# Kernel optimization log

Hardware: AMD Instinct MI355X
Metric: run time of the kernel (lower is better)

The kernel has to match this reference:

```python
import jax, jax.numpy as jnp
import numpy as np

NC = 80          # class_num
THRESH = 0.5     # objectness threshold (forward arg `thresh`)
IOU_T = 0.3      # NMS IoU threshold (utils.nms(boxes_c, 0.3))
K = 512          # fixed candidate budget per image (jit-safe replacement for nonzero)


def _decode(out, t, anchors):
    """_filter + _parse for one scale. out: (B, 3*(5+NC), H, W) -> boxes (B, H*W*3, 6), conf (B, H*W*3).
    Box columns: x1, y1, x2, y2, conf, cls."""
    B, C, H, W = out.shape
    o = out.transpose(0, 2, 3, 1).reshape(B, H, W, 3, 5 + NC)
    txy = jax.nn.sigmoid(o[..., 0:2])          # sigmoid on tx, ty
    conf = jax.nn.sigmoid(o[..., 4])           # sigmoid on objectness
    gy = jnp.arange(H, dtype=out.dtype)[:, None, None]   # grid row index (idxs[:,1])
    gx = jnp.arange(W, dtype=out.dtype)[None, :, None]   # grid col index (idxs[:,2])
    cy = (gy + txy[..., 1]) * t
    cx = (gx + txy[..., 0]) * t
    w = anchors[:, 0] * jnp.exp(o[..., 2])     # anchors broadcast over anchor axis
    h = anchors[:, 1] * jnp.exp(o[..., 3])
    cls = jnp.argmax(o[..., 5:], axis=-1).astype(out.dtype)
    boxes = jnp.stack([cx - w / 2, cy - h / 2, cx + w / 2, cy + h / 2, conf, cls], axis=-1)
    return boxes.reshape(B, -1, 6), conf.reshape(B, -1)


def _iou(b):
    """Pairwise IoU. b: (B, K, 4) -> (B, K, K)."""
    x1, y1, x2, y2 = b[..., 0], b[..., 1], b[..., 2], b[..., 3]
    area = (x2 - x1) * (y2 - y1)
    ix1 = jnp.maximum(x1[:, :, None], x1[:, None, :])
    iy1 = jnp.maximum(y1[:, :, None], y1[:, None, :])
    ix2 = jnp.minimum(x2[:, :, None], x2[:, None, :])
    iy2 = jnp.minimum(y2[:, :, None], y2[:, None, :])
    inter = jnp.maximum(ix2 - ix1, 0.0) * jnp.maximum(iy2 - iy1, 0.0)
    return inter / (area[:, :, None] + area[:, None, :] - inter + 1e-9)


def setup_inputs() -> dict:
    key = jax.random.key(0)
    k1, k2, k3 = jax.random.split(key, 3)
    B, C = 32, 3 * (5 + NC)
    return {
        "out13": jax.random.normal(k1, (B, C, 13, 13), jnp.float32),
        "out26": jax.random.normal(k2, (B, C, 26, 26), jnp.float32),
        "out52": jax.random.normal(k3, (B, C, 52, 52), jnp.float32),
        "anchors13": jnp.array([[116.0, 90.0], [156.0, 198.0], [373.0, 326.0]], jnp.float32),
        "anchors26": jnp.array([[30.0, 61.0], [62.0, 45.0], [59.0, 119.0]], jnp.float32),
        "anchors52": jnp.array([[10.0, 13.0], [16.0, 30.0], [33.0, 23.0]], jnp.float32),
    }


def reference(out13, out26, out52, anchors13, anchors26, anchors52):
    b13, c13 = _decode(out13, 32.0, anchors13)
    b26, c26 = _decode(out26, 16.0, anchors26)
    b52, c52 = _decode(out52, 8.0, anchors52)
    boxes = jnp.concatenate([b13, b26, b52], axis=1)   # (B, N, 6), N = 3549*3
    conf = jnp.concatenate([c13, c26, c52], axis=1)    # (B, N)
    B = boxes.shape[0]

    # threshold filter (conf > thresh) realized as masked top-K (jit-safe nonzero)
    scores = jnp.where(conf > THRESH, conf, -1.0)
    vals, idx = jax.lax.top_k(scores, K)               # sorted descending, as utils.nms expects
    bk = jnp.take_along_axis(boxes, idx[..., None], axis=1)   # (B, K, 6)
    valid = vals > THRESH                              # (B, K)

    # per-class greedy NMS
    iou = _iou(bk[..., :4])                            # (B, K, K)
    same_cls = bk[..., 5][:, :, None] == bk[..., 5][:, None, :]
    suppress = same_cls & (iou > IOU_T)

    def step(keep, i):
        sup_i = jnp.any(keep & suppress[:, i, :], axis=-1)
        keep = keep.at[:, i].set(valid[:, i] & ~sup_i)
        return keep, None

    keep, _ = jax.lax.scan(step, jnp.zeros((B, K), dtype=bool), jnp.arange(K))
    # (B, K, 7): x1, y1, x2, y2, conf, cls, keep_flag
    return jnp.concatenate([bk, keep[..., None].astype(bk.dtype)], axis=-1)
```

## Files before the change

### kernel.cpp

```cpp
#include <hip/hip_runtime.h>
#include <stdint.h>

#define NC13 507
#define NC26 2028
#define NC52 8112
#define NCAND 10647
#define KSEL 512
#define POOLCAP 4096
#define SUPW 17
#define CMW 17

__device__ __forceinline__ unsigned long long cand_key(
    int i, int b,
    const float* __restrict__ in13,
    const float* __restrict__ in26,
    const float* __restrict__ in52)
{
    const float* in; int HW, base;
    if (i < NC13)              { in = in13; HW = 169;  base = 0; }
    else if (i < NC13 + NC26)  { in = in26; HW = 676;  base = NC13; }
    else                       { in = in52; HW = 2704; base = NC13 + NC26; }
    const int within = i - base;
    const int a  = within / HW;
    const int hw = within - a * HW;
    const float xo = in[((size_t)b * 255 + (size_t)a * 85 + 4) * HW + hw];
    const int n = base + hw * 3 + a;
    const unsigned long long low = (unsigned long long)(0x3FFFu - (unsigned)n);
    return (xo > 0.0f)
        ? ((1ull << 63) | ((unsigned long long)__float_as_uint(xo) << 32) | low)
        : low;
}

__global__ __launch_bounds__(1024) void selscore_kernel(
    const float* __restrict__ in13,
    const float* __restrict__ in26,
    const float* __restrict__ in52,
    int* __restrict__ selidx,
    int* __restrict__ selv)
{
    __shared__ unsigned int hist[4096];
    __shared__ unsigned long long pool[POOLCAP];
    __shared__ unsigned int cnt;
    __shared__ unsigned long long sh_prefix;
    __shared__ unsigned long long sh_tmin;
    __shared__ int sh_krem;
    __shared__ int sh_shift;
    __shared__ int sh_break;

    const int b = blockIdx.x;
    const int tid = threadIdx.x;

    if (tid == 0) { sh_prefix = 0; sh_krem = KSEL; sh_shift = 52; sh_break = 0; cnt = 0; }
    __syncthreads();

    while (true) {
        const int shift = sh_shift;
        const unsigned long long prefix = sh_prefix;
        const int krem = sh_krem;
        __syncthreads();
        for (int i = tid; i < 4096; i += 1024) hist[i] = 0;
        __syncthreads();
        for (int i = tid; i < NCAND; i += 1024) {
            const unsigned long long k = cand_key(i, b, in13, in26, in52);
            const bool ok = (shift == 52) || ((k >> (shift + 12)) == prefix);
            if (ok) atomicAdd(&hist[(unsigned)((k >> shift) & 0xFFFull)], 1u);
        }
        __syncthreads();
        if (tid < 64) {
            unsigned int s = 0;
            for (int q = 0; q < 64; ++q) s += hist[tid * 64 + q];
            unsigned int suf = s;
            for (int off = 1; off < 64; off <<= 1) {
                const unsigned int v = __shfl_down(suf, off);
                if (tid + off < 64) suf += v;
            }
            const unsigned long long ball = __ballot(suf >= (unsigned)krem);
            const int lstar = 63 - __clzll(ball);
            const unsigned int base = (lstar < 63) ? __shfl(suf, lstar + 1) : 0u;
            const unsigned int wv = hist[lstar * 64 + (63 - tid)];
            unsigned int pv = wv;
            for (int off = 1; off < 64; off <<= 1) {
                const unsigned int v = __shfl_up(pv, off);
                if (tid >= (unsigned)off) pv += v;
            }
            const unsigned long long b2 = __ballot(base + pv >= (unsigned)krem);
            const int mstar = __ffsll(b2) - 1;
            const unsigned int pvm = __shfl(pv, mstar);
            const unsigned int wvm = __shfl(wv, mstar);
            if (tid == 0) {
                const int dstar = lstar * 64 + (63 - mstar);
                const unsigned long long np = (prefix << 12) | (unsigned long long)dstar;
                const int Albl = (int)(base + pvm - wvm);
                const int Cpool = (KSEL - krem) + Albl + (int)wvm;
                sh_prefix = np;
                sh_krem = krem - Albl;
                if (Cpool <= POOLCAP || shift == 4) {
                    sh_break = 1;
                    sh_tmin = np << shift;
                } else {
                    sh_shift = shift - 12;
                }
            }
        }
        __syncthreads();
        if (sh_break) break;
    }
    const unsigned long long tmin = sh_tmin;

    for (int i = tid; i < NCAND; i += 1024) {
        const unsigned long long k = cand_key(i, b, in13, in26, in52);
        if (k >= tmin) {
            const unsigned int p = atomicAdd(&cnt, 1u);
            if (p < POOLCAP) pool[p] = k;
        }
    }
    __syncthreads();
    const int C = ((int)cnt < POOLCAP) ? (int)cnt : POOLCAP;

    for (int p = tid; p < C; p += 1024) {
        const unsigned long long k = pool[p];
        int r = 0;
        for (int j = 0; j < C; ++j) r += (pool[j] > k) ? 1 : 0;
        if (r < KSEL) {
            const int idx = 0x3FFF - (int)(k & 0x3FFFull);
            selidx[(size_t)b * KSEL + r] = idx;
            selv[(size_t)b * KSEL + r]   = (int)(k >> 63);
        }
    }
}

__device__ __forceinline__ unsigned long long cls_key(float v, int c) {
    unsigned int u = __float_as_uint(v);
    u = (u & 0x80000000u) ? ~u : (u | 0x80000000u);
    return ((unsigned long long)u << 32) | (unsigned long long)(127 - c);
}

__global__ __launch_bounds__(256) void gather_kernel(
    const float* __restrict__ in13,
    const float* __restrict__ in26,
    const float* __restrict__ in52,
    const float* __restrict__ a13,
    const float* __restrict__ a26,
    const float* __restrict__ a52,
    const int* __restrict__ selidx,
    float* __restrict__ bk,
    int* __restrict__ bkC)
{
    const int lane = threadIdx.x & 63;
    const int r = blockIdx.x * 4 + (threadIdx.x >> 6);
    const int b = blockIdx.y;
    const int idx = selidx[(size_t)b * KSEL + r];

    const float* in; const float* anch; int H; float ts; int loc;
    if (idx < NC13)             { in = in13; anch = a13; H = 13; ts = 32.f; loc = idx; }
    else if (idx < NC13 + NC26) { in = in26; anch = a26; H = 26; ts = 16.f; loc = idx - NC13; }
    else                        { in = in52; anch = a52; H = 52; ts = 8.f;  loc = idx - NC13 - NC26; }
    const int W = H, HW = H * W;
    const int hw = loc / 3, a = loc - hw * 3;
    const int h = hw / W,  w = hw - h * W;
    const float* p = in + ((size_t)b * 255 + (size_t)a * 85) * HW + hw;

    const float v0 = p[(size_t)(5 + lane) * HW];
    const float v1 = p[(size_t)(69 + (lane & 15)) * HW];
    const float bc = p[(size_t)(lane % 5) * HW];

    unsigned long long k = cls_key(v0, lane);
    {
        const unsigned long long k1 = cls_key(v1, 64 + (lane & 15));
        if (k1 > k) k = k1;
    }
    #pragma unroll
    for (int off = 32; off; off >>= 1) {
        const unsigned int hi = __shfl_xor((unsigned int)(k >> 32), off);
        const unsigned int lo = __shfl_xor((unsigned int)(k & 0xFFFFFFFFu), off);
        const unsigned long long o = ((unsigned long long)hi << 32) | lo;
        if (o > k) k = o;
    }
    const int cls = 127 - (int)(k & 0x7Full);

    const float tx = __shfl(bc, 0);
    const float ty = __shfl(bc, 1);
    const float tw = __shfl(bc, 2);
    const float th = __shfl(bc, 3);
    const float xo = __shfl(bc, 4);

    if (lane == 0) {
        const float sx   = 1.0f / (1.0f + expf(-tx));
        const float sy   = 1.0f / (1.0f + expf(-ty));
        const float conf = 1.0f / (1.0f + expf(-xo));
        const float cx = ((float)w + sx) * ts;
        const float cy = ((float)h + sy) * ts;
        const float bw = anch[2 * a + 0] * expf(tw);
        const float bh = anch[2 * a + 1] * expf(th);
        float* o = bk + ((size_t)b * KSEL + r) * 6;
        o[0] = cx - bw * 0.5f; o[1] = cy - bh * 0.5f;
        o[2] = cx + bw * 0.5f; o[3] = cy + bh * 0.5f;
        o[4] = conf; o[5] = (float)cls;
        bkC[(size_t)b * KSEL + r] = cls;
    }
}

__global__ __launch_bounds__(512) void nms_kernel(
    const float* __restrict__ bk,
    const int* __restrict__ bkC,
    const int* __restrict__ selv,
    float* __restrict__ out)
{
    __shared__ float X1[KSEL], Y1[KSEL], X2[KSEL], Y2[KSEL], AR[KSEL];
    __shared__ int CLS[KSEL];
    __shared__ unsigned int CM[80 * CMW];
    __shared__ unsigned int SUP[KSEL * SUPW];
    __shared__ unsigned int KEEP[16];
    __shared__ int shV;

    const int b = blockIdx.x;
    const int tid = threadIdx.x;

    const float* src = bk + ((size_t)b * KSEL + tid) * 6;
    const float x1 = src[0], y1 = src[1], x2 = src[2], y2 = src[3];
    const float ar = (x2 - x1) * (y2 - y1);
    const int ci = bkC[(size_t)b * KSEL + tid];
    X1[tid] = x1; Y1[tid] = y1; X2[tid] = x2; Y2[tid] = y2;
    AR[tid] = ar; CLS[tid] = ci;
    const int v = selv[(size_t)b * KSEL + tid];
    if (tid == 0) shV = 0;
    for (int i = tid; i < 80 * CMW; i += KSEL) CM[i] = 0;
    __syncthreads();

    atomicOr(&CM[ci * CMW + (tid >> 5)], 1u << (tid & 31));
    const unsigned long long bal = __ballot(v != 0);
    if ((tid & 63) == 0) atomicAdd(&shV, __popcll(bal));
    __syncthreads();

    for (int wj = 0; wj < 16; ++wj) {
        unsigned int m = CM[ci * CMW + wj];
        unsigned int bits = 0;
        while (m) {
            const int bit = __ffs(m) - 1;
            m &= m - 1;
            const int j = wj * 32 + bit;
            const float iw = fminf(x2, X2[j]) - fmaxf(x1, X1[j]);
            const float ih = fminf(y2, Y2[j]) - fmaxf(y1, Y1[j]);
            if (iw > 0.0f && ih > 0.0f) {
                const float inter = iw * ih;
                if (inter > 0.3f * (ar + AR[j] - inter + 1e-9f))
                    bits |= (1u << bit);
            }
        }
        SUP[tid * SUPW + wj] = bits;
    }
    __syncthreads();

    if (tid < 64) {
        const int V = shV;
        unsigned int keepw = 0;
        unsigned int buf[16];
        #pragma unroll
        for (int r = 0; r < 16; ++r)
            buf[r] = (tid < 16) ? SUP[r * SUPW + tid] : 0u;
        for (int g = 0; g < 32; ++g) {
            unsigned int nbuf[16] = {0};
            if (g < 31) {
                #pragma unroll
                for (int r = 0; r < 16; ++r)
                    nbuf[r] = (tid < 16) ? SUP[((g + 1) * 16 + r) * SUPW + tid] : 0u;
            }
            #pragma unroll
            for (int r = 0; r < 16; ++r) {
                const int i = g * 16 + r;
                const bool anysup = __any((keepw & buf[r]) != 0u);
                const bool ki = (i < V) && !anysup;
                if (ki && tid == (i >> 5)) keepw |= (1u << (i & 31));
            }
            #pragma unroll
            for (int r = 0; r < 16; ++r) buf[r] = nbuf[r];
        }
        if (tid < 16) KEEP[tid] = keepw;
    }
    __syncthreads();

    const float kf = ((KEEP[tid >> 5] >> (tid & 31)) & 1u) ? 1.0f : 0.0f;
    float* dst = out + ((size_t)b * KSEL + tid) * 7;
    dst[0] = src[0]; dst[1] = src[1]; dst[2] = src[2];
    dst[3] = src[3]; dst[4] = src[4]; dst[5] = src[5];
    dst[6] = kf;
}

extern "C" void kernel_launch(void* const* d_in, const int* in_sizes, int n_in,
                              void* d_out, int out_size, void* d_ws, size_t ws_size,
                              hipStream_t stream)
{
    (void)n_in; (void)out_size; (void)ws_size;
    const float* in13 = (const float*)d_in[0];
    const float* in26 = (const float*)d_in[1];
    const float* in52 = (const float*)d_in[2];
    const float* a13  = (const float*)d_in[3];
    const float* a26  = (const float*)d_in[4];
    const float* a52  = (const float*)d_in[5];
    float* out = (float*)d_out;
    const int B = in_sizes[0] / (255 * 169);

    char* w = (char*)d_ws;
    int* selidx = (int*)w;  w += ((size_t)B * KSEL * sizeof(int) + 255) & ~(size_t)255;
    int* selv   = (int*)w;  w += ((size_t)B * KSEL * sizeof(int) + 255) & ~(size_t)255;
    float* bk   = (float*)w; w += ((size_t)B * KSEL * 6 * sizeof(float) + 255) & ~(size_t)255;
    int* bkC    = (int*)w;   w += ((size_t)B * KSEL * sizeof(int) + 255) & ~(size_t)255;

    selscore_kernel<<<dim3(B), 1024, 0, stream>>>(in13, in26, in52, selidx, selv);
    gather_kernel<<<dim3(KSEL / 4, B), 256, 0, stream>>>(
        in13, in26, in52, a13, a26, a52, selidx, bk, bkC);
    nms_kernel<<<dim3(B), 512, 0, stream>>>(bk, bkC, selv, out);
}
```

Before: 85.62 us.

## Decode all candidates densely, then gather selected boxes in NMS kernel

New measurement: 80.30 us. 6.2% less time.

```diff
diff --git a/kernel.cpp b/kernel.cpp
--- a/kernel.cpp
+++ b/kernel.cpp
@@ -129,80 +129,64 @@
     }
 }
 
-__device__ __forceinline__ unsigned long long cls_key(float v, int c) {
-    unsigned int u = __float_as_uint(v);
-    u = (u & 0x80000000u) ? ~u : (u | 0x80000000u);
-    return ((unsigned long long)u << 32) | (unsigned long long)(127 - c);
-}
-
-__global__ __launch_bounds__(256) void gather_kernel(
+__global__ __launch_bounds__(256) void decode_all_kernel(
     const float* __restrict__ in13,
     const float* __restrict__ in26,
     const float* __restrict__ in52,
     const float* __restrict__ a13,
     const float* __restrict__ a26,
     const float* __restrict__ a52,
+    float* __restrict__ boxesAll)
+{
+    const int chunk = blockIdx.x;
+    const int a = blockIdx.y;
+    const int b = blockIdx.z;
+    const float* in; const float* anch; int H, base, hw0; float ts;
+    if (chunk == 0)      { in = in13; anch = a13; H = 13; ts = 32.f; base = 0;           hw0 = 0; }
+    else if (chunk <= 3) { in = in26; anch = a26; H = 26; ts = 16.f; base = NC13;        hw0 = (chunk - 1) * 256; }
+    else                 { in = in52; anch = a52; H = 52; ts = 8.f;  base = NC13 + NC26; hw0 = (chunk - 4) * 256; }
+    const int HW = H * H;
+    const int hw = hw0 + threadIdx.x;
+    if (hw >= HW) return;
+    const int h = hw / H, w = hw - h * H;
+    const float* p = in + ((size_t)b * 255 + (size_t)a * 85) * HW + hw;
+
+    const float tx = p[0];
+    const float ty = p[(size_t)HW];
+    const float tw = p[(size_t)2 * HW];
+    const float th = p[(size_t)3 * HW];
+    const float xo = p[(size_t)4 * HW];
+
+    unsigned long long k = 0;
+    #pragma unroll
+    for (int c = 0; c < 80; ++c) {
+        const float v = p[(size_t)(5 + c) * HW];
+        unsigned int u = __float_as_uint(v);
+        u = (u & 0x80000000u) ? ~u : (u | 0x80000000u);
+        const unsigned long long kk =
+            ((unsigned long long)u << 32) | (unsigned long long)(127 - c);
+        if (kk > k) k = kk;
+    }
+    const int cls = 127 - (int)(k & 0xFFull);
+
+    const float sx   = 1.0f / (1.0f + expf(-tx));
+    const float sy   = 1.0f / (1.0f + expf(-ty));
+    const float conf = 1.0f / (1.0f + expf(-xo));
+    const float cx = ((float)w + sx) * ts;
+    const float cy = ((float)h + sy) * ts;
+    const float bw = anch[2 * a + 0] * expf(tw);
+    const float bh = anch[2 * a + 1] * expf(th);
+
+    const int i = base + a * HW + hw;
+    float* o = boxesAll + ((size_t)b * NCAND + i) * 6;
+    o[0] = cx - bw * 0.5f; o[1] = cy - bh * 0.5f;
+    o[2] = cx + bw * 0.5f; o[3] = cy + bh * 0.5f;
+    o[4] = conf; o[5] = (float)cls;
+}
+
+__global__ __launch_bounds__(512) void nms_kernel(
+    const float* __restrict__ boxesAll,
     const int* __restrict__ selidx,
-    float* __restrict__ bk,
-    int* __restrict__ bkC)
-{
-    const int lane = threadIdx.x & 63;
-    const int r = blockIdx.x * 4 + (threadIdx.x >> 6);
-    const int b = blockIdx.y;
-    const int idx = selidx[(size_t)b * KSEL + r];
-
-    const float* in; const float* anch; int H; float ts; int loc;
-    if (idx < NC13)             { in = in13; anch = a13; H = 13; ts = 32.f; loc = idx; }
-    else if (idx < NC13 + NC26) { in = in26; anch = a26; H = 26; ts = 16.f; loc = idx - NC13; }
-    else                        { in = in52; anch = a52; H = 52; ts = 8.f;  loc = idx - NC13 - NC26; }
-    const int W = H, HW = H * W;
-    const int hw = loc / 3, a = loc - hw * 3;
-    const int h = hw / W,  w = hw - h * W;
-    const float* p = in + ((size_t)b * 255 + (size_t)a * 85) * HW + hw;
-
-    const float v0 = p[(size_t)(5 + lane) * HW];
-    const float v1 = p[(size_t)(69 + (lane & 15)) * HW];
-    const float bc = p[(size_t)(lane % 5) * HW];
-
-    unsigned long long k = cls_key(v0, lane);
-    {
-        const unsigned long long k1 = cls_key(v1, 64 + (lane & 15));
-        if (k1 > k) k = k1;
-    }
-    #pragma unroll
-    for (int off = 32; off; off >>= 1) {
-        const unsigned int hi = __shfl_xor((unsigned int)(k >> 32), off);
-        const unsigned int lo = __shfl_xor((unsigned int)(k & 0xFFFFFFFFu), off);
-        const unsigned long long o = ((unsigned long long)hi << 32) | lo;
-        if (o > k) k = o;
-    }
-    const int cls = 127 - (int)(k & 0x7Full);
-
-    const float tx = __shfl(bc, 0);
-    const float ty = __shfl(bc, 1);
-    const float tw = __shfl(bc, 2);
-    const float th = __shfl(bc, 3);
-    const float xo = __shfl(bc, 4);
-
-    if (lane == 0) {
-        const float sx   = 1.0f / (1.0f + expf(-tx));
-        const float sy   = 1.0f / (1.0f + expf(-ty));
-        const float conf = 1.0f / (1.0f + expf(-xo));
-        const float cx = ((float)w + sx) * ts;
-        const float cy = ((float)h + sy) * ts;
-        const float bw = anch[2 * a + 0] * expf(tw);
-        const float bh = anch[2 * a + 1] * expf(th);
-        float* o = bk + ((size_t)b * KSEL + r) * 6;
-        o[0] = cx - bw * 0.5f; o[1] = cy - bh * 0.5f;
-        o[2] = cx + bw * 0.5f; o[3] = cy + bh * 0.5f;
-        o[4] = conf; o[5] = (float)cls;
-        bkC[(size_t)b * KSEL + r] = cls;
-    }
-}
-
-__global__ __launch_bounds__(512) void nms_kernel(
-    const float* __restrict__ bk,
-    const int* __restrict__ bkC,
     const int* __restrict__ selv,
     float* __restrict__ out)
 {
@@ -216,15 +200,24 @@
     const int b = blockIdx.x;
     const int tid = threadIdx.x;
 
-    const float* src = bk + ((size_t)b * KSEL + tid) * 6;
+    const int n = selidx[(size_t)b * KSEL + tid];
+    int base, HW;
+    if (n < NC13)             { base = 0;           HW = 169; }
+    else if (n < NC13 + NC26) { base = NC13;        HW = 676; }
+    else                      { base = NC13 + NC26; HW = 2704; }
+    const int within = n - base;
+    const int hw = within / 3, a = within - 3 * hw;
+    const int i = base + a * HW + hw;
+    const float* src = boxesAll + ((size_t)b * NCAND + i) * 6;
     const float x1 = src[0], y1 = src[1], x2 = src[2], y2 = src[3];
+    const float conf = src[4], clsf = src[5];
     const float ar = (x2 - x1) * (y2 - y1);
-    const int ci = bkC[(size_t)b * KSEL + tid];
+    const int ci = (int)clsf;
     X1[tid] = x1; Y1[tid] = y1; X2[tid] = x2; Y2[tid] = y2;
     AR[tid] = ar; CLS[tid] = ci;
     const int v = selv[(size_t)b * KSEL + tid];
     if (tid == 0) shV = 0;
-    for (int i = tid; i < 80 * CMW; i += KSEL) CM[i] = 0;
+    for (int q = tid; q < 80 * CMW; q += KSEL) CM[q] = 0;
     __syncthreads();
 
     atomicOr(&CM[ci * CMW + (tid >> 5)], 1u << (tid & 31));
@@ -267,10 +260,10 @@
             }
             #pragma unroll
             for (int r = 0; r < 16; ++r) {
-                const int i = g * 16 + r;
+                const int ii = g * 16 + r;
                 const bool anysup = __any((keepw & buf[r]) != 0u);
-                const bool ki = (i < V) && !anysup;
-                if (ki && tid == (i >> 5)) keepw |= (1u << (i & 31));
+                const bool ki = (ii < V) && !anysup;
+                if (ki && tid == (ii >> 5)) keepw |= (1u << (ii & 31));
             }
             #pragma unroll
             for (int r = 0; r < 16; ++r) buf[r] = nbuf[r];
@@ -281,8 +274,8 @@
 
     const float kf = ((KEEP[tid >> 5] >> (tid & 31)) & 1u) ? 1.0f : 0.0f;
     float* dst = out + ((size_t)b * KSEL + tid) * 7;
-    dst[0] = src[0]; dst[1] = src[1]; dst[2] = src[2];
-    dst[3] = src[3]; dst[4] = src[4]; dst[5] = src[5];
+    dst[0] = x1; dst[1] = y1; dst[2] = x2;
+    dst[3] = y2; dst[4] = conf; dst[5] = clsf;
     dst[6] = kf;
 }
 
@@ -303,11 +296,11 @@
     char* w = (char*)d_ws;
     int* selidx = (int*)w;  w += ((size_t)B * KSEL * sizeof(int) + 255) & ~(size_t)255;
     int* selv   = (int*)w;  w += ((size_t)B * KSEL * sizeof(int) + 255) & ~(size_t)255;
-    float* bk   = (float*)w; w += ((size_t)B * KSEL * 6 * sizeof(float) + 255) & ~(size_t)255;
-    int* bkC    = (int*)w;   w += ((size_t)B * KSEL * sizeof(int) + 255) & ~(size_t)255;
+    float* boxesAll = (float*)w;
+    w += ((size_t)B * NCAND * 6 * sizeof(float) + 255) & ~(size_t)255;
 
     selscore_kernel<<<dim3(B), 1024, 0, stream>>>(in13, in26, in52, selidx, selv);
-    gather_kernel<<<dim3(KSEL / 4, B), 256, 0, stream>>>(
-        in13, in26, in52, a13, a26, a52, selidx, bk, bkC);
-    nms_kernel<<<dim3(B), 512, 0, stream>>>(bk, bkC, selv, out);
-}
+    decode_all_kernel<<<dim3(15, 3, B), 256, 0, stream>>>(
+        in13, in26, in52, a13, a26, a52, boxesAll);
+    nms_kernel<<<dim3(B), 512, 0, stream>>>(boxesAll, selidx, selv, out);
+}
```

## Precompute keys, geometry and top-level histogram in a wide grid kernel

Applied to the files above, without the earlier changes.

Measured after the change: 94.95 us. 1.11x slower.

```diff
diff --git a/kernel.cpp b/kernel.cpp
--- a/kernel.cpp
+++ b/kernel.cpp
@@ -5,70 +5,131 @@
 #define NC26 2028
 #define NC52 8112
 #define NCAND 10647
+#define NCANDP 10648
+#define PB13 0
+#define PB26 508
+#define PB52 2536
 #define KSEL 512
-#define POOLCAP 4096
+#define POOLCAP 768
+#define POOLTGT 640
 #define SUPW 17
 #define CMW 17
-
-__device__ __forceinline__ unsigned long long cand_key(
-    int i, int b,
-    const float* __restrict__ in13,
-    const float* __restrict__ in26,
-    const float* __restrict__ in52)
-{
-    const float* in; int HW, base;
-    if (i < NC13)              { in = in13; HW = 169;  base = 0; }
-    else if (i < NC13 + NC26)  { in = in26; HW = 676;  base = NC13; }
-    else                       { in = in52; HW = 2704; base = NC13 + NC26; }
-    const int within = i - base;
-    const int a  = within / HW;
-    const int hw = within - a * HW;
-    const float xo = in[((size_t)b * 255 + (size_t)a * 85 + 4) * HW + hw];
-    const int n = base + hw * 3 + a;
+#define HBINS 4096
+
+__device__ __forceinline__ unsigned long long make_key(float xo, int n) {
     const unsigned long long low = (unsigned long long)(0x3FFFu - (unsigned)n);
     return (xo > 0.0f)
         ? ((1ull << 63) | ((unsigned long long)__float_as_uint(xo) << 32) | low)
         : low;
 }
 
-__global__ __launch_bounds__(1024) void selscore_kernel(
+__global__ __launch_bounds__(256) void lightscore_kernel(
     const float* __restrict__ in13,
     const float* __restrict__ in26,
     const float* __restrict__ in52,
+    const float* __restrict__ a13,
+    const float* __restrict__ a26,
+    const float* __restrict__ a52,
+    float* __restrict__ geo,
+    unsigned long long* __restrict__ keys,
+    unsigned int* __restrict__ hist)
+{
+    __shared__ unsigned int lh[HBINS];
+    const int tid = threadIdx.x;
+    const int b = blockIdx.y;
+    for (int q = tid; q < HBINS; q += 256) lh[q] = 0;
+    __syncthreads();
+
+    const int i = blockIdx.x * 256 + tid;
+    if (i < NCANDP) {
+        if (i == 507) {
+            keys[(size_t)b * NCANDP + 507] = 0ull;
+        } else {
+            const float* in; const float* anch; int HW, Hdim, pb, nb; float ts;
+            if (i < 507)       { in = in13; anch = a13; HW = 169;  Hdim = 13; ts = 32.f; pb = PB13; nb = 0; }
+            else if (i < 2536) { in = in26; anch = a26; HW = 676;  Hdim = 26; ts = 16.f; pb = PB26; nb = NC13; }
+            else               { in = in52; anch = a52; HW = 2704; Hdim = 52; ts = 8.f;  pb = PB52; nb = NC13 + NC26; }
+            const int wi = i - pb;
+            const int a = wi / HW, hw = wi - a * HW;
+            const int h = hw / Hdim, w = hw - h * Hdim;
+            const float* p = in + ((size_t)b * 255 + (size_t)a * 85) * HW + hw;
+            const float tx = p[0];
+            const float ty = p[(size_t)HW];
+            const float tw = p[(size_t)2 * HW];
+            const float th = p[(size_t)3 * HW];
+            const float xo = p[(size_t)4 * HW];
+            const int n = nb + hw * 3 + a;
+            const unsigned long long k = make_key(xo, n);
+            keys[(size_t)b * NCANDP + i] = k;
+            if (xo > 0.f) atomicAdd(&lh[(unsigned)(k >> 52)], 1u);
+            const float sx = 1.0f / (1.0f + expf(-tx));
+            const float sy = 1.0f / (1.0f + expf(-ty));
+            const float cf = 1.0f / (1.0f + expf(-xo));
+            const float cx = ((float)w + sx) * ts;
+            const float cy = ((float)h + sy) * ts;
+            const float bw = anch[2 * a] * expf(tw);
+            const float bh = anch[2 * a + 1] * expf(th);
+            float* g = geo + (size_t)b * 5 * NCANDP;
+            g[(size_t)0 * NCANDP + i] = cx - bw * 0.5f;
+            g[(size_t)1 * NCANDP + i] = cy - bh * 0.5f;
+            g[(size_t)2 * NCANDP + i] = cx + bw * 0.5f;
+            g[(size_t)3 * NCANDP + i] = cy + bh * 0.5f;
+            g[(size_t)4 * NCANDP + i] = cf;
+        }
+    }
+    __syncthreads();
+    unsigned int* hb = hist + (size_t)b * HBINS;
+    for (int q = tid; q < HBINS; q += 256) {
+        const unsigned int v = lh[q];
+        if (v) atomicAdd(&hb[q], v);
+    }
+}
+
+struct SelS {
+    unsigned int hist[HBINS];
+    unsigned long long pool[POOLCAP];
+};
+
+__global__ __launch_bounds__(1024) void selgather_kernel(
+    const unsigned long long* __restrict__ keys,
+    const unsigned int* __restrict__ hist,
     int* __restrict__ selidx,
-    int* __restrict__ selv)
-{
-    __shared__ unsigned int hist[4096];
-    __shared__ unsigned long long pool[POOLCAP];
-    __shared__ unsigned int cnt;
-    __shared__ unsigned long long sh_prefix;
-    __shared__ unsigned long long sh_tmin;
-    __shared__ int sh_krem;
-    __shared__ int sh_shift;
-    __shared__ int sh_break;
+    int* __restrict__ selV)
+{
+    __shared__ __align__(16) SelS S;
+    __shared__ unsigned long long sh_prefix, sh_tmin;
+    __shared__ int sh_krem, sh_shift, sh_brk, sh_V;
+    __shared__ unsigned int sh_cnt;
 
     const int b = blockIdx.x;
     const int tid = threadIdx.x;
-
-    if (tid == 0) { sh_prefix = 0; sh_krem = KSEL; sh_shift = 52; sh_break = 0; cnt = 0; }
+    const unsigned long long* kb = keys + (size_t)b * NCANDP;
+
+    {
+        const unsigned int* gh = hist + (size_t)b * HBINS;
+        for (int i = tid; i < HBINS; i += 1024) S.hist[i] = gh[i];
+    }
+    if (tid == 0) { sh_cnt = 0; sh_prefix = 0; sh_krem = KSEL; sh_shift = 52; sh_brk = 0; }
+    __syncthreads();
+
+    if (tid < 64) {
+        unsigned int s = 0;
+        for (int q = 0; q < 64; ++q) s += S.hist[tid * 64 + q];
+        #pragma unroll
+        for (int off = 32; off; off >>= 1) s += __shfl_xor(s, off);
+        if (tid == 0) sh_V = (int)s;
+    }
+    __syncthreads();
+    if (tid == 0 && sh_V < KSEL) S.hist[0] += (unsigned)(NCAND - sh_V);
     __syncthreads();
 
     while (true) {
         const int shift = sh_shift;
         const unsigned long long prefix = sh_prefix;
         const int krem = sh_krem;
-        __syncthreads();
-        for (int i = tid; i < 4096; i += 1024) hist[i] = 0;
-        __syncthreads();
-        for (int i = tid; i < NCAND; i += 1024) {
-            const unsigned long long k = cand_key(i, b, in13, in26, in52);
-            const bool ok = (shift == 52) || ((k >> (shift + 12)) == prefix);
-            if (ok) atomicAdd(&hist[(unsigned)((k >> shift) & 0xFFFull)], 1u);
-        }
-        __syncthreads();
         if (tid < 64) {
             unsigned int s = 0;
-            for (int q = 0; q < 64; ++q) s += hist[tid * 64 + q];
+            for (int q = 0; q < 64; ++q) s += S.hist[tid * 64 + q];
             unsigned int suf = s;
             for (int off = 1; off < 64; off <<= 1) {
                 const unsigned int v = __shfl_down(suf, off);
@@ -77,7 +138,7 @@
             const unsigned long long ball = __ballot(suf >= (unsigned)krem);
             const int lstar = 63 - __clzll(ball);
             const unsigned int base = (lstar < 63) ? __shfl(suf, lstar + 1) : 0u;
-            const unsigned int wv = hist[lstar * 64 + (63 - tid)];
+            const unsigned int wv = S.hist[lstar * 64 + (63 - tid)];
             unsigned int pv = wv;
             for (int off = 1; off < 64; off <<= 1) {
                 const unsigned int v = __shfl_up(pv, off);
@@ -94,8 +155,8 @@
                 const int Cpool = (KSEL - krem) + Albl + (int)wvm;
                 sh_prefix = np;
                 sh_krem = krem - Albl;
-                if (Cpool <= POOLCAP || shift == 4) {
-                    sh_break = 1;
+                if (Cpool <= POOLTGT || shift == 4) {
+                    sh_brk = 1;
                     sh_tmin = np << shift;
                 } else {
                     sh_shift = shift - 12;
@@ -103,30 +164,38 @@
             }
         }
         __syncthreads();
-        if (sh_break) break;
+        if (sh_brk) break;
+
+        const int nshift = sh_shift;
+        const unsigned long long nprefix = sh_prefix;
+        for (int i = tid; i < HBINS; i += 1024) S.hist[i] = 0;
+        __syncthreads();
+        for (int i = tid; i < NCANDP; i += 1024) {
+            const unsigned long long k = kb[i];
+            if ((k >> (nshift + 12)) == nprefix)
+                atomicAdd(&S.hist[(unsigned)((k >> nshift) & 0xFFFull)], 1u);
+        }
+        __syncthreads();
     }
     const unsigned long long tmin = sh_tmin;
 
-    for (int i = tid; i < NCAND; i += 1024) {
-        const unsigned long long k = cand_key(i, b, in13, in26, in52);
+    for (int i = tid; i < NCANDP; i += 1024) {
+        const unsigned long long k = kb[i];
         if (k >= tmin) {
-            const unsigned int p = atomicAdd(&cnt, 1u);
-            if (p < POOLCAP) pool[p] = k;
-        }
-    }
-    __syncthreads();
-    const int C = ((int)cnt < POOLCAP) ? (int)cnt : POOLCAP;
+            const unsigned int p = atomicAdd(&sh_cnt, 1u);
+            if (p < POOLCAP) S.pool[p] = k;
+        }
+    }
+    __syncthreads();
+    const int C = ((int)sh_cnt < POOLCAP) ? (int)sh_cnt : POOLCAP;
 
     for (int p = tid; p < C; p += 1024) {
-        const unsigned long long k = pool[p];
+        const unsigned long long k = S.pool[p];
         int r = 0;
-        for (int j = 0; j < C; ++j) r += (pool[j] > k) ? 1 : 0;
-        if (r < KSEL) {
-            const int idx = 0x3FFF - (int)(k & 0x3FFFull);
-            selidx[(size_t)b * KSEL + r] = idx;
-            selv[(size_t)b * KSEL + r]   = (int)(k >> 63);
-        }
-    }
+        for (int j = 0; j < C; ++j) r += (S.pool[j] > k) ? 1 : 0;
+        if (r < KSEL) selidx[(size_t)b * KSEL + r] = 0x3FFF - (int)(k & 0x3FFFull);
+    }
+    if (tid == 0) selV[b] = sh_V;
 }
 
 __device__ __forceinline__ unsigned long long cls_key(float v, int c) {
@@ -135,34 +204,27 @@
     return ((unsigned long long)u << 32) | (unsigned long long)(127 - c);
 }
 
-__global__ __launch_bounds__(256) void gather_kernel(
+__global__ __launch_bounds__(256) void clsgather_kernel(
     const float* __restrict__ in13,
     const float* __restrict__ in26,
     const float* __restrict__ in52,
-    const float* __restrict__ a13,
-    const float* __restrict__ a26,
-    const float* __restrict__ a52,
     const int* __restrict__ selidx,
-    float* __restrict__ bk,
-    int* __restrict__ bkC)
+    int* __restrict__ clsArr)
 {
     const int lane = threadIdx.x & 63;
     const int r = blockIdx.x * 4 + (threadIdx.x >> 6);
     const int b = blockIdx.y;
-    const int idx = selidx[(size_t)b * KSEL + r];
-
-    const float* in; const float* anch; int H; float ts; int loc;
-    if (idx < NC13)             { in = in13; anch = a13; H = 13; ts = 32.f; loc = idx; }
-    else if (idx < NC13 + NC26) { in = in26; anch = a26; H = 26; ts = 16.f; loc = idx - NC13; }
-    else                        { in = in52; anch = a52; H = 52; ts = 8.f;  loc = idx - NC13 - NC26; }
-    const int W = H, HW = H * W;
-    const int hw = loc / 3, a = loc - hw * 3;
-    const int h = hw / W,  w = hw - h * W;
+    const int n = selidx[(size_t)b * KSEL + r];
+
+    const float* in; int HW, loc;
+    if (n < NC13)             { in = in13; HW = 169;  loc = n; }
+    else if (n < NC13 + NC26) { in = in26; HW = 676;  loc = n - NC13; }
+    else                      { in = in52; HW = 2704; loc = n - NC13 - NC26; }
+    const int hw = loc / 3, a = loc - 3 * hw;
     const float* p = in + ((size_t)b * 255 + (size_t)a * 85) * HW + hw;
 
     const float v0 = p[(size_t)(5 + lane) * HW];
     const float v1 = p[(size_t)(69 + (lane & 15)) * HW];
-    const float bc = p[(size_t)(lane % 5) * HW];
 
     unsigned long long k = cls_key(v0, lane);
     {
@@ -176,60 +238,48 @@
         const unsigned long long o = ((unsigned long long)hi << 32) | lo;
         if (o > k) k = o;
     }
-    const int cls = 127 - (int)(k & 0x7Full);
-
-    const float tx = __shfl(bc, 0);
-    const float ty = __shfl(bc, 1);
-    const float tw = __shfl(bc, 2);
-    const float th = __shfl(bc, 3);
-    const float xo = __shfl(bc, 4);
-
-    if (lane == 0) {
-        const float sx   = 1.0f / (1.0f + expf(-tx));
-        const float sy   = 1.0f / (1.0f + expf(-ty));
-        const float conf = 1.0f / (1.0f + expf(-xo));
-        const float cx = ((float)w + sx) * ts;
-        const float cy = ((float)h + sy) * ts;
-        const float bw = anch[2 * a + 0] * expf(tw);
-        const float bh = anch[2 * a + 1] * expf(th);
-        float* o = bk + ((size_t)b * KSEL + r) * 6;
-        o[0] = cx - bw * 0.5f; o[1] = cy - bh * 0.5f;
-        o[2] = cx + bw * 0.5f; o[3] = cy + bh * 0.5f;
-        o[4] = conf; o[5] = (float)cls;
-        bkC[(size_t)b * KSEL + r] = cls;
-    }
+    if (lane == 0) clsArr[(size_t)b * KSEL + r] = 127 - (int)(k & 0x7Full);
 }
 
 __global__ __launch_bounds__(512) void nms_kernel(
-    const float* __restrict__ bk,
-    const int* __restrict__ bkC,
-    const int* __restrict__ selv,
+    const float* __restrict__ geo,
+    const int* __restrict__ clsArr,
+    const int* __restrict__ selidx,
+    const int* __restrict__ selV,
     float* __restrict__ out)
 {
     __shared__ float X1[KSEL], Y1[KSEL], X2[KSEL], Y2[KSEL], AR[KSEL];
-    __shared__ int CLS[KSEL];
     __shared__ unsigned int CM[80 * CMW];
     __shared__ unsigned int SUP[KSEL * SUPW];
     __shared__ unsigned int KEEP[16];
-    __shared__ int shV;
 
     const int b = blockIdx.x;
     const int tid = threadIdx.x;
 
-    const float* src = bk + ((size_t)b * KSEL + tid) * 6;
-    const float x1 = src[0], y1 = src[1], x2 = src[2], y2 = src[3];
+    const int n = selidx[(size_t)b * KSEL + tid];
+    int pb, HW, nb;
+    if (n < NC13)             { pb = PB13; HW = 169;  nb = 0; }
+    else if (n < NC13 + NC26) { pb = PB26; HW = 676;  nb = NC13; }
+    else                      { pb = PB52; HW = 2704; nb = NC13 + NC26; }
+    const int loc = n - nb;
+    const int hw = loc / 3, a = loc - 3 * hw;
+    const int i = pb + a * HW + hw;
+
+    const float* g = geo + (size_t)b * 5 * NCANDP;
+    const float x1 = g[(size_t)0 * NCANDP + i];
+    const float y1 = g[(size_t)1 * NCANDP + i];
+    const float x2 = g[(size_t)2 * NCANDP + i];
+    const float y2 = g[(size_t)3 * NCANDP + i];
+    const float cf = g[(size_t)4 * NCANDP + i];
+    const int ci = clsArr[(size_t)b * KSEL + tid];
     const float ar = (x2 - x1) * (y2 - y1);
-    const int ci = bkC[(size_t)b * KSEL + tid];
-    X1[tid] = x1; Y1[tid] = y1; X2[tid] = x2; Y2[tid] = y2;
-    AR[tid] = ar; CLS[tid] = ci;
-    const int v = selv[(size_t)b * KSEL + tid];
-    if (tid == 0) shV = 0;
-    for (int i = tid; i < 80 * CMW; i += KSEL) CM[i] = 0;
+    X1[tid] = x1; Y1[tid] = y1; X2[tid] = x2; Y2[tid] = y2; AR[tid] = ar;
+    for (int q = tid; q < 80 * CMW; q += KSEL) CM[q] = 0;
+    const int V0 = selV[b];
+    const int V = (V0 < KSEL) ? V0 : KSEL;
     __syncthreads();
 
     atomicOr(&CM[ci * CMW + (tid >> 5)], 1u << (tid & 31));
-    const unsigned long long bal = __ballot(v != 0);
-    if ((tid & 63) == 0) atomicAdd(&shV, __popcll(bal));
     __syncthreads();
 
     for (int wj = 0; wj < 16; ++wj) {
@@ -252,28 +302,27 @@
     __syncthreads();
 
     if (tid < 64) {
-        const int V = shV;
         unsigned int keepw = 0;
         unsigned int buf[16];
         #pragma unroll
-        for (int r = 0; r < 16; ++r)
-            buf[r] = (tid < 16) ? SUP[r * SUPW + tid] : 0u;
-        for (int g = 0; g < 32; ++g) {
+        for (int q = 0; q < 16; ++q)
+            buf[q] = (tid < 16) ? SUP[q * SUPW + tid] : 0u;
+        for (int gg = 0; gg < 32; ++gg) {
             unsigned int nbuf[16] = {0};
-            if (g < 31) {
+            if (gg < 31) {
                 #pragma unroll
-                for (int r = 0; r < 16; ++r)
-                    nbuf[r] = (tid < 16) ? SUP[((g + 1) * 16 + r) * SUPW + tid] : 0u;
+                for (int q = 0; q < 16; ++q)
+                    nbuf[q] = (tid < 16) ? SUP[((gg + 1) * 16 + q) * SUPW + tid] : 0u;
             }
             #pragma unroll
-            for (int r = 0; r < 16; ++r) {
-                const int i = g * 16 + r;
-                const bool anysup = __any((keepw & buf[r]) != 0u);
-                const bool ki = (i < V) && !anysup;
-                if (ki && tid == (i >> 5)) keepw |= (1u << (i & 31));
+            for (int q = 0; q < 16; ++q) {
+                const int ii = gg * 16 + q;
+                const bool anysup = __any((keepw & buf[q]) != 0u);
+                const bool ki = (ii < V) && !anysup;
+                if (ki && tid == (ii >> 5)) keepw |= (1u << (ii & 31));
             }
             #pragma unroll
-            for (int r = 0; r < 16; ++r) buf[r] = nbuf[r];
+            for (int q = 0; q < 16; ++q) buf[q] = nbuf[q];
         }
         if (tid < 16) KEEP[tid] = keepw;
     }
@@ -281,9 +330,8 @@
 
     const float kf = ((KEEP[tid >> 5] >> (tid & 31)) & 1u) ? 1.0f : 0.0f;
     float* dst = out + ((size_t)b * KSEL + tid) * 7;
-    dst[0] = src[0]; dst[1] = src[1]; dst[2] = src[2];
-    dst[3] = src[3]; dst[4] = src[4]; dst[5] = src[5];
-    dst[6] = kf;
+    dst[0] = x1; dst[1] = y1; dst[2] = x2; dst[3] = y2;
+    dst[4] = cf; dst[5] = (float)ci; dst[6] = kf;
 }
 
 extern "C" void kernel_launch(void* const* d_in, const int* in_sizes, int n_in,
@@ -301,13 +349,21 @@
     const int B = in_sizes[0] / (255 * 169);
 
     char* w = (char*)d_ws;
+    unsigned long long* keys = (unsigned long long*)w;
+    w += ((size_t)B * NCANDP * sizeof(unsigned long long) + 255) & ~(size_t)255;
+    float* geo = (float*)w;
+    w += ((size_t)B * 5 * NCANDP * sizeof(float) + 255) & ~(size_t)255;
+    unsigned int* hist = (unsigned int*)w;
+    w += ((size_t)B * HBINS * sizeof(unsigned int) + 255) & ~(size_t)255;
     int* selidx = (int*)w;  w += ((size_t)B * KSEL * sizeof(int) + 255) & ~(size_t)255;
-    int* selv   = (int*)w;  w += ((size_t)B * KSEL * sizeof(int) + 255) & ~(size_t)255;
-    float* bk   = (float*)w; w += ((size_t)B * KSEL * 6 * sizeof(float) + 255) & ~(size_t)255;
-    int* bkC    = (int*)w;   w += ((size_t)B * KSEL * sizeof(int) + 255) & ~(size_t)255;
-
-    selscore_kernel<<<dim3(B), 1024, 0, stream>>>(in13, in26, in52, selidx, selv);
-    gather_kernel<<<dim3(KSEL / 4, B), 256, 0, stream>>>(
-        in13, in26, in52, a13, a26, a52, selidx, bk, bkC);
-    nms_kernel<<<dim3(B), 512, 0, stream>>>(bk, bkC, selv, out);
-}
+    int* selV   = (int*)w;  w += ((size_t)B * sizeof(int) + 255) & ~(size_t)255;
+    int* clsArr = (int*)w;  w += ((size_t)B * KSEL * sizeof(int) + 255) & ~(size_t)255;
+
+    hipMemsetAsync(hist, 0, (size_t)B * HBINS * sizeof(unsigned int), stream);
+    lightscore_kernel<<<dim3((NCANDP + 255) / 256, B), 256, 0, stream>>>(
+        in13, in26, in52, a13, a26, a52, geo, keys, hist);
+    selgather_kernel<<<dim3(B), 1024, 0, stream>>>(keys, hist, selidx, selV);
+    clsgather_kernel<<<dim3(KSEL / 4, B), 256, 0, stream>>>(
+        in13, in26, in52, selidx, clsArr);
+    nms_kernel<<<dim3(B), 512, 0, stream>>>(geo, clsArr, selidx, selV, out);
+}
```
